# Performance work log

Measured on AMD Instinct MI355X. Metric: run time of the kernel, lower is better.

## Reference

```python
import jax, jax.numpy as jnp
import numpy as np

B, L, DIM = 2, 4096, 512
HEADS, KS = 8, 33
HEAD_DIM = DIM // HEADS
SCALE = HEAD_DIM ** -0.5


def setup_inputs() -> dict:
    key = jax.random.key(0)
    ks = jax.random.split(key, 5)
    s = 0.02
    return {
        "x": jax.random.normal(ks[0], (B, L, DIM), dtype=jnp.float32),
        "w_qkv": jax.random.normal(ks[1], (3 * DIM, DIM), dtype=jnp.float32) * s,
        "b_qkv": jax.random.normal(ks[2], (3 * DIM,), dtype=jnp.float32) * s,
        "w_proj": jax.random.normal(ks[3], (DIM, DIM), dtype=jnp.float32) * s,
        "b_proj": jax.random.normal(ks[4], (DIM,), dtype=jnp.float32) * s,
    }


def _na1d(q, k, v):
    # q,k,v: [B, L, H, d]. Each query i attends to KS tokens whose window
    # start is clamp(i - KS//2, 0, L-KS) (NATTEN boundary-clamped neighborhood).
    starts = jnp.clip(jnp.arange(L) - KS // 2, 0, L - KS)          # [L]
    idx = starts[:, None] + jnp.arange(KS)[None, :]                # [L, KS]
    k_g = k[:, idx]                                                # [B, L, KS, H, d]
    v_g = v[:, idx]                                                # [B, L, KS, H, d]
    scores = jnp.einsum("blhd,blkhd->bhlk", q * SCALE, k_g)        # [B, H, L, KS]
    attn = jax.nn.softmax(scores, axis=-1)
    out = jnp.einsum("bhlk,blkhd->blhd", attn, v_g)                # [B, L, H, d]
    return out


def reference(x, w_qkv, b_qkv, w_proj, b_proj):
    qkv = x @ w_qkv.T + b_qkv                                      # [B, L, 3*DIM]
    qkv = qkv.reshape(B, L, 3, HEADS, HEAD_DIM)
    q, k, v = qkv[:, :, 0], qkv[:, :, 1], qkv[:, :, 2]
    out = _na1d(q, k, v).reshape(B, L, DIM)
    return out @ w_proj.T + b_proj
```

## Files before the change

kernel.cpp:

```cpp
#include <hip/hip_runtime.h>
#include <hip/hip_bf16.h>

#define B_ 2
#define L_ 4096
#define DIM_ 512
#define HEADS_ 8
#define HDIM_ 64
#define KS_ 33

typedef __bf16 bf16;
typedef __bf16 bf16x4 __attribute__((ext_vector_type(4)));
typedef __bf16 bf16x8 __attribute__((ext_vector_type(8)));
typedef float f32x4 __attribute__((ext_vector_type(4)));

__global__ void cvt_to_bf16(const float* __restrict__ src, bf16* __restrict__ dst,
                            int n)
{
    int i = blockIdx.x * blockDim.x + threadIdx.x;
    if (i < n) dst[i] = (bf16)src[i];
}

template <typename OutT>
__global__ __launch_bounds__(256)
void gemm_nt_bias(const bf16* __restrict__ A, const bf16* __restrict__ W,
                  const bf16* __restrict__ bias, OutT* __restrict__ C,
                  int M, int N, int K)
{
    __shared__ bf16 As[128][72];
    __shared__ bf16 Bs[128][72];

    const int tid  = threadIdx.x;
    const int wave = tid >> 6;
    const int lane = tid & 63;
    const int wm   = (wave >> 1) * 64;
    const int wn   = (wave & 1) * 64;
    const int l16  = lane & 15;
    const int quad = lane >> 4;

    const int row0 = blockIdx.x * 128;
    const int col0 = blockIdx.y * 128;

    f32x4 acc[4][4] = {};

    for (int k0 = 0; k0 < K; k0 += 64) {
        #pragma unroll
        for (int it = 0; it < 4; ++it) {
            int idx = it * 256 + tid;
            int r   = idx >> 3;
            int c   = (idx & 7) * 8;
            *(bf16x8*)(&As[r][c]) =
                *(const bf16x8*)(&A[(size_t)(row0 + r) * K + k0 + c]);
            *(bf16x8*)(&Bs[r][c]) =
                *(const bf16x8*)(&W[(size_t)(col0 + r) * K + k0 + c]);
        }
        __syncthreads();

        #pragma unroll
        for (int ks = 0; ks < 2; ++ks) {
            bf16x8 af[4], bfr[4];
            #pragma unroll
            for (int i = 0; i < 4; ++i) {
                af[i]  = *(const bf16x8*)(&As[wm + i * 16 + l16][ks * 32 + quad * 8]);
                bfr[i] = *(const bf16x8*)(&Bs[wn + i * 16 + l16][ks * 32 + quad * 8]);
            }
            #pragma unroll
            for (int mi = 0; mi < 4; ++mi)
                #pragma unroll
                for (int ni = 0; ni < 4; ++ni)
                    acc[mi][ni] = __builtin_amdgcn_mfma_f32_16x16x32_bf16(
                        af[mi], bfr[ni], acc[mi][ni], 0, 0, 0);
        }
        __syncthreads();
    }

    #pragma unroll
    for (int ni = 0; ni < 4; ++ni) {
        int n = col0 + wn + ni * 16 + l16;
        float bv = (float)bias[n];
        #pragma unroll
        for (int mi = 0; mi < 4; ++mi) {
            int mrow = row0 + wm + mi * 16 + quad * 4;
            #pragma unroll
            for (int r = 0; r < 4; ++r)
                C[(size_t)(mrow + r) * N + n] = (OutT)(acc[mi][ni][r] + bv);
        }
    }
}

__global__ __launch_bounds__(256)
void na1d_attn_mfma(const bf16* __restrict__ qkv, bf16* __restrict__ att)
{
    __shared__ bf16 Plds[4][16][72];

    const int wave = threadIdx.x >> 6;
    const int lane = threadIdx.x & 63;
    const int l16  = lane & 15;
    const int quad = lane >> 4;

    const int wid = blockIdx.x * 4 + wave;
    const int qg  = wid & 255;
    const int bh  = wid >> 8;
    const int h   = bh & 7;
    const int b   = bh >> 3;
    const int q0  = qg * 16;

    int k_base = q0 - 16;
    if (k_base < 0) k_base = 0;
    if (k_base > L_ - KS_) k_base = L_ - KS_;

    const size_t rs = 3 * DIM_;

    const bf16* qptr = qkv + (size_t)(b * L_ + q0 + l16) * rs + h * HDIM_ + quad * 8;
    bf16x8 qf0 = *(const bf16x8*)(qptr);
    bf16x8 qf1 = *(const bf16x8*)(qptr + 32);

    const bf16* kcol = qkv + (size_t)(b * L_ + k_base) * rs + DIM_ + h * HDIM_;
    f32x4 s[3] = {};
    #pragma unroll
    for (int t = 0; t < 3; ++t) {
        const bf16* kptr = kcol + (size_t)(t * 16 + l16) * rs + quad * 8;
        bf16x8 kf0 = *(const bf16x8*)(kptr);
        bf16x8 kf1 = *(const bf16x8*)(kptr + 32);
        s[t] = __builtin_amdgcn_mfma_f32_16x16x32_bf16(qf0, kf0, s[t], 0, 0, 0);
        s[t] = __builtin_amdgcn_mfma_f32_16x16x32_bf16(qf1, kf1, s[t], 0, 0, 0);
    }

    int offr[4];
    #pragma unroll
    for (int r = 0; r < 4; ++r) {
        int lq = q0 + quad * 4 + r;
        int st = lq - KS_ / 2;
        if (st < 0) st = 0;
        if (st > L_ - KS_) st = L_ - KS_;
        offr[r] = st - k_base;
    }
    float sv[3][4];
    #pragma unroll
    for (int t = 0; t < 3; ++t) {
        int j = t * 16 + l16;
        #pragma unroll
        for (int r = 0; r < 4; ++r) {
            float x = s[t][r] * 0.125f;
            sv[t][r] = (j >= offr[r] && j <= offr[r] + 32) ? x : -1e30f;
        }
    }

    float mr[4], sum[4];
    #pragma unroll
    for (int r = 0; r < 4; ++r)
        mr[r] = fmaxf(fmaxf(sv[0][r], sv[1][r]), sv[2][r]);
    #pragma unroll
    for (int o = 1; o < 16; o <<= 1)
        #pragma unroll
        for (int r = 0; r < 4; ++r)
            mr[r] = fmaxf(mr[r], __shfl_xor(mr[r], o, 64));
    #pragma unroll
    for (int t = 0; t < 3; ++t)
        #pragma unroll
        for (int r = 0; r < 4; ++r)
            sv[t][r] = __expf(sv[t][r] - mr[r]);
    #pragma unroll
    for (int r = 0; r < 4; ++r)
        sum[r] = sv[0][r] + sv[1][r] + sv[2][r];
    #pragma unroll
    for (int o = 1; o < 16; o <<= 1)
        #pragma unroll
        for (int r = 0; r < 4; ++r)
            sum[r] += __shfl_xor(sum[r], o, 64);
    #pragma unroll
    for (int r = 0; r < 4; ++r) {
        float inv = 1.0f / sum[r];
        #pragma unroll
        for (int t = 0; t < 3; ++t) sv[t][r] *= inv;
    }

    bf16* P = &Plds[wave][0][0];
    {
        int rr = lane >> 2;
        int c0 = 48 + (lane & 3) * 4;
        *(bf16x4*)(&P[rr * 72 + c0]) = (bf16x4){(bf16)0.f, (bf16)0.f, (bf16)0.f, (bf16)0.f};
    }
    #pragma unroll
    for (int t = 0; t < 3; ++t)
        #pragma unroll
        for (int r = 0; r < 4; ++r)
            P[(quad * 4 + r) * 72 + t * 16 + l16] = (bf16)sv[t][r];
    __syncthreads();

    bf16x8 pf0 = *(const bf16x8*)(&P[l16 * 72 + quad * 8]);
    bf16x8 pf1 = *(const bf16x8*)(&P[l16 * 72 + 32 + quad * 8]);

    const bf16* vcol = qkv + (size_t)(b * L_ + k_base) * rs + 2 * DIM_ + h * HDIM_;
    f32x4 o[4] = {};
    #pragma unroll
    for (int t = 0; t < 4; ++t) {
        bf16x8 vf0, vf1;
        #pragma unroll
        for (int j = 0; j < 8; ++j) {
            vf0[j] = vcol[(size_t)(quad * 8 + j) * rs + t * 16 + l16];
            vf1[j] = vcol[(size_t)(32 + quad * 8 + j) * rs + t * 16 + l16];
        }
        o[t] = __builtin_amdgcn_mfma_f32_16x16x32_bf16(pf0, vf0, o[t], 0, 0, 0);
        o[t] = __builtin_amdgcn_mfma_f32_16x16x32_bf16(pf1, vf1, o[t], 0, 0, 0);
    }

    bf16* orow = att + (size_t)(b * L_ + q0) * DIM_ + h * HDIM_;
    #pragma unroll
    for (int t = 0; t < 4; ++t)
        #pragma unroll
        for (int r = 0; r < 4; ++r)
            orow[(size_t)(quad * 4 + r) * DIM_ + t * 16 + l16] = (bf16)o[t][r];
}

extern "C" void kernel_launch(void* const* d_in, const int* in_sizes, int n_in,
                              void* d_out, int out_size, void* d_ws, size_t ws_size,
                              hipStream_t stream) {
    const int n_x  = B_ * L_ * DIM_;
    const int n_wq = 3 * DIM_ * DIM_;
    const int n_bq = 3 * DIM_;
    const int n_wp = DIM_ * DIM_;
    const int n_bp = DIM_;

    char* ws = (char*)d_ws;
    bf16* xb  = (bf16*)ws;
    bf16* wqb = xb  + n_x;
    bf16* bqb = wqb + n_wq;
    bf16* wpb = bqb + n_bq;
    bf16* bpb = wpb + n_wp;
    bf16* qkv = bpb + n_bp;
    bf16* att = qkv + (size_t)8192 * 1536;

    float* out = (float*)d_out;
    const int M = B_ * L_;

    cvt_to_bf16<<<(n_x  + 255) / 256, 256, 0, stream>>>((const float*)d_in[0], xb,  n_x);
    cvt_to_bf16<<<(n_wq + 255) / 256, 256, 0, stream>>>((const float*)d_in[1], wqb, n_wq);
    cvt_to_bf16<<<(n_bq + 255) / 256, 256, 0, stream>>>((const float*)d_in[2], bqb, n_bq);
    cvt_to_bf16<<<(n_wp + 255) / 256, 256, 0, stream>>>((const float*)d_in[3], wpb, n_wp);
    cvt_to_bf16<<<(n_bp + 255) / 256, 256, 0, stream>>>((const float*)d_in[4], bpb, n_bp);

    gemm_nt_bias<bf16><<<dim3(M / 128, (3 * DIM_) / 128), 256, 0, stream>>>(
        xb, wqb, bqb, qkv, M, 3 * DIM_, DIM_);

    na1d_attn_mfma<<<dim3((B_ * HEADS_ * L_) / 64), 256, 0, stream>>>(qkv, att);

    gemm_nt_bias<float><<<dim3(M / 128, DIM_ / 128), 256, 0, stream>>>(
        att, wpb, bpb, out, M, DIM_, DIM_);
}
```

Baseline: 135.4 us.

## Fuse bf16 conversions into one kernel and use async global-to-LDS swizzled GEMM loads

The five separate fp32-to-bf16 conversion launches become a single vectorized kernel that picks its source and destination tensor from the block index, writing 8 elements per thread. The GEMM tile loads now use global_load_lds direct copies into unpadded LDS tiles. An XOR swizzle on the 16-byte column chunks replaces the padding as the way to avoid bank conflicts on the MFMA fragment reads. This targets launch overhead and register round-trips on the staging path, but relies on the compiler inserting correct waits for the asynchronous LDS writes and on the per-lane LDS addresses being contiguous.

```diff
diff --git a/kernel.cpp b/kernel.cpp
--- a/kernel.cpp
+++ b/kernel.cpp
@@ -13,11 +13,38 @@
 typedef __bf16 bf16x8 __attribute__((ext_vector_type(8)));
 typedef float f32x4 __attribute__((ext_vector_type(4)));
 
-__global__ void cvt_to_bf16(const float* __restrict__ src, bf16* __restrict__ dst,
-                            int n)
-{
-    int i = blockIdx.x * blockDim.x + threadIdx.x;
-    if (i < n) dst[i] = (bf16)src[i];
+typedef __attribute__((address_space(3))) void lds_void;
+typedef __attribute__((address_space(1))) const void glb_void;
+
+__device__ __forceinline__ void async_cp16(const bf16* g, bf16* l)
+{
+    __builtin_amdgcn_global_load_lds((glb_void*)g, (lds_void*)l, 16, 0, 0);
+}
+
+__global__ __launch_bounds__(256)
+void cvt_all(const float* __restrict__ x,  const float* __restrict__ wq,
+             const float* __restrict__ bq, const float* __restrict__ wp,
+             const float* __restrict__ bp,
+             bf16* __restrict__ xb,  bf16* __restrict__ wqb,
+             bf16* __restrict__ bqb, bf16* __restrict__ wpb,
+             bf16* __restrict__ bpb)
+{
+    const int blk = blockIdx.x;
+    const float* src; bf16* dst; int n, base;
+    if (blk < 2048)       { src = x;  dst = xb;  n = 4194304; base = blk; }
+    else if (blk < 2432)  { src = wq; dst = wqb; n = 786432;  base = blk - 2048; }
+    else if (blk < 2560)  { src = wp; dst = wpb; n = 262144;  base = blk - 2432; }
+    else if (blk == 2560) { src = bq; dst = bqb; n = 1536;    base = 0; }
+    else                  { src = bp; dst = bpb; n = 512;     base = 0; }
+    int i = base * 2048 + threadIdx.x * 8;
+    if (i + 8 <= n) {
+        float4 a = *(const float4*)(src + i);
+        float4 b = *(const float4*)(src + i + 4);
+        bf16x8 o;
+        o[0] = (bf16)a.x; o[1] = (bf16)a.y; o[2] = (bf16)a.z; o[3] = (bf16)a.w;
+        o[4] = (bf16)b.x; o[5] = (bf16)b.y; o[6] = (bf16)b.z; o[7] = (bf16)b.w;
+        *(bf16x8*)(dst + i) = o;
+    }
 }
 
 template <typename OutT>
@@ -26,8 +53,8 @@
                   const bf16* __restrict__ bias, OutT* __restrict__ C,
                   int M, int N, int K)
 {
-    __shared__ bf16 As[128][72];
-    __shared__ bf16 Bs[128][72];
+    __shared__ bf16 As[128][64];
+    __shared__ bf16 Bs[128][64];
 
     const int tid  = threadIdx.x;
     const int wave = tid >> 6;
@@ -45,13 +72,11 @@
     for (int k0 = 0; k0 < K; k0 += 64) {
         #pragma unroll
         for (int it = 0; it < 4; ++it) {
-            int idx = it * 256 + tid;
-            int r   = idx >> 3;
-            int c   = (idx & 7) * 8;
-            *(bf16x8*)(&As[r][c]) =
-                *(const bf16x8*)(&A[(size_t)(row0 + r) * K + k0 + c]);
-            *(bf16x8*)(&Bs[r][c]) =
-                *(const bf16x8*)(&W[(size_t)(col0 + r) * K + k0 + c]);
+            int f   = it * 256 + tid;
+            int r   = f >> 3;
+            int c8l = (f & 7) ^ (r & 7);
+            async_cp16(&A[(size_t)(row0 + r) * K + k0 + c8l * 8], &As[r][(f & 7) * 8]);
+            async_cp16(&W[(size_t)(col0 + r) * K + k0 + c8l * 8], &Bs[r][(f & 7) * 8]);
         }
         __syncthreads();
 
@@ -60,8 +85,10 @@
             bf16x8 af[4], bfr[4];
             #pragma unroll
             for (int i = 0; i < 4; ++i) {
-                af[i]  = *(const bf16x8*)(&As[wm + i * 16 + l16][ks * 32 + quad * 8]);
-                bfr[i] = *(const bf16x8*)(&Bs[wn + i * 16 + l16][ks * 32 + quad * 8]);
+                int ra = wm + i * 16 + l16;
+                int rb = wn + i * 16 + l16;
+                af[i]  = *(const bf16x8*)(&As[ra][((ks * 4 + quad) ^ (ra & 7)) * 8]);
+                bfr[i] = *(const bf16x8*)(&Bs[rb][((ks * 4 + quad) ^ (rb & 7)) * 8]);
             }
             #pragma unroll
             for (int mi = 0; mi < 4; ++mi)
@@ -233,11 +260,10 @@
     float* out = (float*)d_out;
     const int M = B_ * L_;
 
-    cvt_to_bf16<<<(n_x  + 255) / 256, 256, 0, stream>>>((const float*)d_in[0], xb,  n_x);
-    cvt_to_bf16<<<(n_wq + 255) / 256, 256, 0, stream>>>((const float*)d_in[1], wqb, n_wq);
-    cvt_to_bf16<<<(n_bq + 255) / 256, 256, 0, stream>>>((const float*)d_in[2], bqb, n_bq);
-    cvt_to_bf16<<<(n_wp + 255) / 256, 256, 0, stream>>>((const float*)d_in[3], wpb, n_wp);
-    cvt_to_bf16<<<(n_bp + 255) / 256, 256, 0, stream>>>((const float*)d_in[4], bpb, n_bp);
+    cvt_all<<<2562, 256, 0, stream>>>(
+        (const float*)d_in[0], (const float*)d_in[1], (const float*)d_in[2],
+        (const float*)d_in[3], (const float*)d_in[4],
+        xb, wqb, bqb, wpb, bpb);
 
     gemm_nt_bias<bf16><<<dim3(M / 128, (3 * DIM_) / 128), 256, 0, stream>>>(
         xb, wqb, bqb, qkv, M, 3 * DIM_, DIM_);
```

New measurement: 125.7 us. 7.2% less time.
